# Kernel tuning notes

Hardware: AMD Instinct MI355X
Metric: run time of the kernel (lower is better)

Reference implementation:

```python
import jax, jax.numpy as jnp
import numpy as np

# Static multi-level feature-map shapes (H, W) per level.
SPATIAL_SHAPES = np.array([[92, 160], [46, 80], [23, 40], [12, 20]], dtype=np.int32)
NUM_HEADS = 8
NUM_LEVELS = 4
NUM_POINTS = 4      # sampling points per head per level (num_all_points)
NUM_Z = 4           # num_Z_anchors; NUM_POINTS % NUM_Z == 0
EMBED = 256
HEAD_DIM = EMBED // NUM_HEADS


def setup_inputs() -> dict:
    key = jax.random.key(0)
    ks = jax.random.split(key, 10)
    bs, nq = 2, 10000
    nv = int((SPATIAL_SHAPES[:, 0] * SPATIAL_SHAPES[:, 1]).sum())  # 19560
    query = jax.random.normal(ks[0], (bs, nq, EMBED), jnp.float32)
    value = jax.random.normal(ks[1], (bs, nv, EMBED), jnp.float32)
    query_pos = jax.random.normal(ks[2], (bs, nq, EMBED), jnp.float32)
    reference_points = jax.random.uniform(ks[3], (bs, nq, NUM_Z, 2), jnp.float32)
    W_val = jax.random.normal(ks[4], (EMBED, EMBED), jnp.float32) / jnp.sqrt(EMBED)
    b_val = jnp.zeros((EMBED,), jnp.float32)
    W_off = jax.random.normal(ks[5], (EMBED, NUM_HEADS * NUM_LEVELS * NUM_POINTS * 2), jnp.float32) * 0.01
    b_off = jax.random.normal(ks[6], (NUM_HEADS * NUM_LEVELS * NUM_POINTS * 2,), jnp.float32) * 0.5
    W_attn = jax.random.normal(ks[7], (EMBED, NUM_HEADS * NUM_LEVELS * NUM_POINTS), jnp.float32) * 0.02
    b_attn = jnp.zeros((NUM_HEADS * NUM_LEVELS * NUM_POINTS,), jnp.float32)
    spatial_shapes = jnp.asarray(SPATIAL_SHAPES)
    return {
        'query': query, 'value': value, 'query_pos': query_pos,
        'reference_points': reference_points,
        'W_val': W_val, 'b_val': b_val, 'W_off': W_off, 'b_off': b_off,
        'W_attn': W_attn, 'b_attn': b_attn, 'spatial_shapes': spatial_shapes,
    }


def _bilinear(v, x, y, H, W):
    """grid_sample(mode='bilinear', padding_mode='zeros', align_corners=False).

    v: (bs, H, W, heads, d); x, y: (bs, nq, heads, P) pixel coords.
    Returns (bs, nq, heads, P, d).
    """
    x0 = jnp.floor(x)
    y0 = jnp.floor(y)
    wx1 = x - x0
    wy1 = y - y0
    wx0 = 1.0 - wx1
    wy0 = 1.0 - wy1
    x0i = x0.astype(jnp.int32)
    y0i = y0.astype(jnp.int32)
    b = jnp.arange(v.shape[0])[:, None, None, None]
    h = jnp.arange(v.shape[3])[None, None, :, None]

    def gather(yi, xi):
        valid = (yi >= 0) & (yi < H) & (xi >= 0) & (xi < W)
        yc = jnp.clip(yi, 0, H - 1)
        xc = jnp.clip(xi, 0, W - 1)
        g = v[b, yc, xc, h]  # (bs, nq, heads, P, d)
        return g * valid[..., None].astype(v.dtype)

    return (gather(y0i, x0i) * (wy0 * wx0)[..., None]
            + gather(y0i, x0i + 1) * (wy0 * wx1)[..., None]
            + gather(y0i + 1, x0i) * (wy1 * wx0)[..., None]
            + gather(y0i + 1, x0i + 1) * (wy1 * wx1)[..., None])


def reference(query, value, query_pos, reference_points, W_val, b_val,
              W_off, b_off, W_attn, b_attn, spatial_shapes):
    bs, nq, _ = query.shape
    q = query + query_pos
    # value projection -> per-head values
    v = (value @ W_val + b_val).reshape(bs, -1, NUM_HEADS, HEAD_DIM)
    # sampling offsets and attention weights from query
    off = (q @ W_off + b_off).reshape(bs, nq, NUM_HEADS, NUM_LEVELS, NUM_POINTS, 2)
    attn = (q @ W_attn + b_attn).reshape(bs, nq, NUM_HEADS, NUM_LEVELS * NUM_POINTS)
    attn = jax.nn.softmax(attn, axis=-1).reshape(bs, nq, NUM_HEADS, NUM_LEVELS, NUM_POINTS)
    # normalize offsets by (w, h) of each level
    norm = jnp.stack([spatial_shapes[:, 1], spatial_shapes[:, 0]], -1).astype(q.dtype)  # (L, 2)
    off = off / norm[None, None, None, :, None, :]
    # fold Z-anchor reference points in, matching the shape[-1]==2 branch
    off = off.reshape(bs, nq, NUM_HEADS, NUM_LEVELS, NUM_POINTS // NUM_Z, NUM_Z, 2)
    loc = reference_points[:, :, None, None, None, :, :] + off
    loc = loc.reshape(bs, nq, NUM_HEADS, NUM_LEVELS, NUM_POINTS, 2)
    grid = 2.0 * loc - 1.0  # grid_sample convention

    start = 0
    sampled = []
    for lvl in range(NUM_LEVELS):
        H, W = int(SPATIAL_SHAPES[lvl, 0]), int(SPATIAL_SHAPES[lvl, 1])
        vl = v[:, start:start + H * W].reshape(bs, H, W, NUM_HEADS, HEAD_DIM)
        start += H * W
        # align_corners=False pixel coords
        x = ((grid[:, :, :, lvl, :, 0] + 1.0) * W - 1.0) * 0.5
        y = ((grid[:, :, :, lvl, :, 1] + 1.0) * H - 1.0) * 0.5
        sampled.append(_bilinear(vl, x, y, H, W))
    samp = jnp.stack(sampled, axis=3)  # (bs, nq, heads, L, P, d)
    out = (samp * attn[..., None]).sum(axis=(3, 4))  # (bs, nq, heads, d)
    return out.reshape(bs, nq, NUM_HEADS * HEAD_DIM)
```

## Files before the change

kernel.cpp:

```cpp
#include <hip/hip_runtime.h>
#include <hip/hip_fp16.h>

#define NQ 10000
#define BS 2
#define NV 19560
#define NH 8
#define HD 32
#define EMB 256

typedef __attribute__((ext_vector_type(8))) short bf16x8;
typedef __attribute__((ext_vector_type(4))) float f32x4;
typedef __attribute__((ext_vector_type(4))) short s16x4;

__device__ __forceinline__ unsigned short f2bf(float x) {
    unsigned u = __float_as_uint(x);
    u += 0x7FFFu + ((u >> 16) & 1u);
    return (unsigned short)(u >> 16);
}

__global__ __launch_bounds__(256) void convert_W(
    const float* __restrict__ Wv, const float* __restrict__ Wo,
    const float* __restrict__ Wa, const float* __restrict__ bv,
    const float* __restrict__ bo, const float* __restrict__ ba,
    ushort* __restrict__ Bt, float* __restrict__ bias) {
    int n = blockIdx.x;
    int k = threadIdx.x;
    float x;
    if (n < 256)       x = Wv[k * 256 + n];
    else if (n < 512)  x = Wo[k * 256 + (n - 256)];
    else               x = Wa[k * 128 + (n - 512)];
    Bt[n * 256 + k] = f2bf(x);
    if (k == 0)
        bias[n] = (n < 256) ? bv[n] : (n < 512) ? bo[n - 256] : ba[n - 512];
}

__global__ __launch_bounds__(256) void gemm_fused(
    const float* __restrict__ value, const float* __restrict__ query,
    const float* __restrict__ qpos, const ushort* __restrict__ Bt,
    const float* __restrict__ bias,
    ushort* __restrict__ Cv, float* __restrict__ C0, float* __restrict__ C1)
{
    __shared__ short As[64][40], Bhs[128][40];

    const int tid = threadIdx.x;

    const int bid0 = blockIdx.x;
    int bid;
    if (bid0 < 1224) {
        bid = (bid0 & 7) * 153 + (bid0 >> 3);
    } else {
        int q = bid0 - 1224;
        int xcd = q & 7, idx = q >> 3;
        int orig = (xcd < 3) ? (xcd * 118 + idx)
                             : (3 * 118 + (xcd - 3) * 117 + idx);
        bid = 1224 + orig;
    }

    bool isval; int mblk, npan;
    if (bid < 1224) { isval = true;  mblk = bid >> 1; npan = bid & 1; }
    else { int q = bid - 1224; isval = false; mblk = q / 3; npan = q % 3; }

    const int M  = isval ? (BS * NV) : (BS * NQ);
    const int m0 = mblk * 64;
    const int n0 = npan * 128;
    const int nbase = (isval ? 0 : 256) + n0;

    const float* A = isval ? value : query;

    const int arow = tid >> 2;
    const int acol = (tid & 3) * 8;
    const bool aval = (m0 + arow) < M;
    const float* Ap  = A    + (size_t)(m0 + arow) * 256 + acol;
    const float* A2p = qpos + (size_t)(m0 + arow) * 256 + acol;
    const int brow = tid >> 1;
    const int bcol = (tid & 1) * 16;
    const ushort* Bp = Bt + (size_t)(nbase + brow) * 256 + bcol;

    const int lane = tid & 63, wave = tid >> 6;
    const int wrow = (wave >> 1) * 32, wcol = (wave & 1) * 64;
    const int lr = lane & 15, quad = lane >> 4, lk = quad * 8;

    f32x4 acc[2][4] = {};

    for (int k0 = 0; k0 < 256; k0 += 32) {
        #pragma unroll
        for (int g = 0; g < 2; g++) {
            f32x4 v = {};
            if (aval) {
                v = *(const f32x4*)(Ap + k0 + g * 4);
                if (!isval) v += *(const f32x4*)(A2p + k0 + g * 4);
            }
            s16x4 hh;
            #pragma unroll
            for (int e = 0; e < 4; e++) hh[e] = (short)f2bf(v[e]);
            *(s16x4*)&As[arow][acol + g * 4] = hh;
        }
        *(bf16x8*)&Bhs[brow][bcol]     = *(const bf16x8*)(Bp + k0);
        *(bf16x8*)&Bhs[brow][bcol + 8] = *(const bf16x8*)(Bp + k0 + 8);
        __syncthreads();

        bf16x8 af[2], bhf[4];
        #pragma unroll
        for (int i = 0; i < 2; i++)
            af[i] = *(const bf16x8*)&As[wrow + i * 16 + lr][lk];
        #pragma unroll
        for (int j = 0; j < 4; j++)
            bhf[j] = *(const bf16x8*)&Bhs[wcol + j * 16 + lr][lk];
        #pragma unroll
        for (int i = 0; i < 2; i++)
            #pragma unroll
            for (int j = 0; j < 4; j++)
                acc[i][j] = __builtin_amdgcn_mfma_f32_16x16x32_bf16(af[i], bhf[j], acc[i][j], 0, 0, 0);
        __syncthreads();
    }

    #pragma unroll
    for (int j = 0; j < 4; j++) {
        int cc = wcol + j * 16 + lr;
        int col = n0 + cc;
        float bb = bias[nbase + cc];
        #pragma unroll
        for (int i = 0; i < 2; i++) {
            int gmb = m0 + wrow + i * 16 + quad * 4;
            #pragma unroll
            for (int r = 0; r < 4; r++) {
                int gm = gmb + r;
                if (gm < M) {
                    float val = acc[i][j][r] + bb;
                    if (isval) {
                        int h = col >> 5, d = col & 31;
                        int b = (gm >= NV) ? 1 : 0;
                        int pix = gm - b * NV;
                        Cv[((size_t)(b * 8 + h) * NV + pix) * 32 + d] =
                            __half_as_ushort(__float2half(val));
                    } else {
                        if (col < 256) C0[(size_t)gm * 256 + col] = val;
                        else           C1[(size_t)gm * 128 + (col - 256)] = val;
                    }
                }
            }
        }
    }
}

__global__ __launch_bounds__(256) void sample4(
    const ushort* __restrict__ v, const float* __restrict__ off,
    const float* __restrict__ attn, const float* __restrict__ refp,
    float* __restrict__ out)
{
    __shared__ int2 s_ow[256][4];

    const int t = threadIdx.x;
    const int combo = blockIdx.x & 15;
    const int qgrp  = blockIdx.x >> 4;
    const int b  = combo & 1;
    const int h0 = combo >> 1;

    {
        const int qloc = t >> 4;
        const int lp   = t & 15;
        const int l = lp >> 2, p = lp & 3;
        const size_t bq = (size_t)b * NQ + qgrp * 16 + qloc;

        float logit = attn[bq * 128 + h0 * 16 + lp];
        float mx = logit;
        #pragma unroll
        for (int m = 1; m < 16; m <<= 1) mx = fmaxf(mx, __shfl_xor(mx, m, 16));
        float e = __expf(logit - mx);
        float s = e;
        #pragma unroll
        for (int m = 1; m < 16; m <<= 1) s += __shfl_xor(s, m, 16);
        float w = e / s;

        const float Wf[4] = {160.f, 80.f, 40.f, 20.f};
        const float Hf[4] = {92.f, 46.f, 23.f, 12.f};
        const int   Wi[4] = {160, 80, 40, 20};
        const int   Hi[4] = {92, 46, 23, 12};
        const int   st[4] = {0, 14720, 18400, 19320};

        float ox = off[bq * 256 + h0 * 32 + l * 8 + p * 2];
        float oy = off[bq * 256 + h0 * 32 + l * 8 + p * 2 + 1];
        float rx = refp[bq * 8 + p * 2];
        float ry = refp[bq * 8 + p * 2 + 1];
        float x = rx * Wf[l] + ox - 0.5f;
        float y = ry * Hf[l] + oy - 0.5f;
        float x0f = floorf(x), y0f = floorf(y);
        float wx1 = x - x0f, wy1 = y - y0f;
        float wx0 = 1.f - wx1, wy0 = 1.f - wy1;
        int x0 = (int)x0f, y0 = (int)y0f;
        const int W = Wi[l], H = Hi[l];
        float mx0 = ((unsigned)x0       < (unsigned)W) ? 1.f : 0.f;
        float mx1 = ((unsigned)(x0 + 1) < (unsigned)W) ? 1.f : 0.f;
        float my0 = ((unsigned)y0       < (unsigned)H) ? 1.f : 0.f;
        float my1 = ((unsigned)(y0 + 1) < (unsigned)H) ? 1.f : 0.f;
        int xc0 = min(max(x0, 0), W - 1);
        int xc1 = min(max(x0 + 1, 0), W - 1);
        int yc0 = min(max(y0, 0), H - 1);
        int yc1 = min(max(y0 + 1, 0), H - 1);
        int base = ((b * 8 + h0) * NV + st[l]) * 32;
        s_ow[t][0] = make_int2(base + (yc0 * W + xc0) * 32,
                               __float_as_int(w * wy0 * wx0 * my0 * mx0));
        s_ow[t][1] = make_int2(base + (yc0 * W + xc1) * 32,
                               __float_as_int(w * wy0 * wx1 * my0 * mx1));
        s_ow[t][2] = make_int2(base + (yc1 * W + xc0) * 32,
                               __float_as_int(w * wy1 * wx0 * my1 * mx0));
        s_ow[t][3] = make_int2(base + (yc1 * W + xc1) * 32,
                               __float_as_int(w * wy1 * wx1 * my1 * mx1));
    }
    __syncthreads();

    const int g = t >> 4;
    const int lane = t & 15;
    const size_t bq = (size_t)b * NQ + qgrp * 16 + g;
    const int d2 = lane * 2;
    const int pbase = g * 16;

    float acc0 = 0.f, acc1 = 0.f, acc2 = 0.f, acc3 = 0.f;
    #pragma unroll
    for (int ib = 0; ib < 4; ib++) {
        int o[16]; float wgt[16];
        #pragma unroll
        for (int pp = 0; pp < 4; pp++) {
            int idx = pbase + ib * 4 + pp;
            #pragma unroll
            for (int c = 0; c < 4; c++) {
                int2 ow = s_ow[idx][c];
                o[pp * 4 + c]   = ow.x;
                wgt[pp * 4 + c] = __int_as_float(ow.y);
            }
        }
        unsigned u[16];
        #pragma unroll
        for (int j = 0; j < 16; j++)
            u[j] = *(const unsigned*)(v + o[j] + d2);
        #pragma unroll
        for (int j = 0; j < 16; j += 2) {
            float2 fa = __half22float2(*(const __half2*)&u[j]);
            float2 fb = __half22float2(*(const __half2*)&u[j + 1]);
            acc0 += wgt[j]     * fa.x;
            acc1 += wgt[j]     * fa.y;
            acc2 += wgt[j + 1] * fb.x;
            acc3 += wgt[j + 1] * fb.y;
        }
    }
    float2 res = make_float2(acc0 + acc2, acc1 + acc3);
    *(float2*)(out + bq * 256 + h0 * 32 + d2) = res;
}

extern "C" void kernel_launch(void* const* d_in, const int* in_sizes, int n_in,
                              void* d_out, int out_size, void* d_ws, size_t ws_size,
                              hipStream_t stream) {
    const float* query     = (const float*)d_in[0];
    const float* value     = (const float*)d_in[1];
    const float* query_pos = (const float*)d_in[2];
    const float* refp      = (const float*)d_in[3];
    const float* W_val     = (const float*)d_in[4];
    const float* b_val     = (const float*)d_in[5];
    const float* W_off     = (const float*)d_in[6];
    const float* b_off     = (const float*)d_in[7];
    const float* W_attn    = (const float*)d_in[8];
    const float* b_attn    = (const float*)d_in[9];
    float* out = (float*)d_out;

    char* w = (char*)d_ws;
    float*  off    = (float*)w;   w += 20480000;
    float*  attn   = (float*)w;   w += 10240000;
    ushort* vp_bf  = (ushort*)w;  w += 20029440;
    ushort* Bt     = (ushort*)w;  w += 327680;
    float*  bias_c = (float*)w;   w += 2560;

    convert_W<<<640, 256, 0, stream>>>(W_val, W_off, W_attn, b_val, b_off, b_attn,
                                       Bt, bias_c);

    gemm_fused<<<1224 + 939, 256, 0, stream>>>(value, query, query_pos, Bt, bias_c,
                                               vp_bf, off, attn);

    sample4<<<(BS * NQ / 16) * NH, 256, 0, stream>>>(vp_bf, off, attn, refp, out);
}
```

Before: 202.5 us.

## Remap sampling kernel to 64 queries per block with 16-byte gathers

The sampling kernel now gives each block 64 queries for one (batch, head) pair instead of 16. Each query gets 4 threads, and each thread handles one level's setup and 8 channels of the head dimension. Value gathers become 16-byte vector loads instead of 4-byte loads, and the setup uses vectorized float4 loads of logits, offsets and reference points. The shared table is padded to 65 columns to avoid bank conflicts, and a tail guard is added because 10000 is not a multiple of 64. In exchange, each thread issues more sequential gathers (64 points) and uses more registers.

```diff
diff --git a/kernel.cpp b/kernel.cpp
--- a/kernel.cpp
+++ b/kernel.cpp
@@ -9,6 +9,7 @@
 #define EMB 256
 
 typedef __attribute__((ext_vector_type(8))) short bf16x8;
+typedef __attribute__((ext_vector_type(8))) unsigned short u16x8;
 typedef __attribute__((ext_vector_type(4))) float f32x4;
 typedef __attribute__((ext_vector_type(4))) short s16x4;
 
@@ -148,7 +149,7 @@
     const float* __restrict__ attn, const float* __restrict__ refp,
     float* __restrict__ out)
 {
-    __shared__ int2 s_ow[256][4];
+    __shared__ int2 s_ow[64][65];
 
     const int t = threadIdx.x;
     const int combo = blockIdx.x & 15;
@@ -156,95 +157,112 @@
     const int b  = combo & 1;
     const int h0 = combo >> 1;
 
+    const int q = t >> 2;
+    const int l = t & 3;
+    const int qt = qgrp * 64 + q;
+    const bool valid = qt < NQ;
+    const size_t bq = (size_t)b * NQ + (valid ? qt : NQ - 1);
+
     {
-        const int qloc = t >> 4;
-        const int lp   = t & 15;
-        const int l = lp >> 2, p = lp & 3;
-        const size_t bq = (size_t)b * NQ + qgrp * 16 + qloc;
-
-        float logit = attn[bq * 128 + h0 * 16 + lp];
-        float mx = logit;
-        #pragma unroll
-        for (int m = 1; m < 16; m <<= 1) mx = fmaxf(mx, __shfl_xor(mx, m, 16));
-        float e = __expf(logit - mx);
-        float s = e;
-        #pragma unroll
-        for (int m = 1; m < 16; m <<= 1) s += __shfl_xor(s, m, 16);
-        float w = e / s;
-
-        const float Wf[4] = {160.f, 80.f, 40.f, 20.f};
-        const float Hf[4] = {92.f, 46.f, 23.f, 12.f};
-        const int   Wi[4] = {160, 80, 40, 20};
-        const int   Hi[4] = {92, 46, 23, 12};
-        const int   st[4] = {0, 14720, 18400, 19320};
-
-        float ox = off[bq * 256 + h0 * 32 + l * 8 + p * 2];
-        float oy = off[bq * 256 + h0 * 32 + l * 8 + p * 2 + 1];
-        float rx = refp[bq * 8 + p * 2];
-        float ry = refp[bq * 8 + p * 2 + 1];
-        float x = rx * Wf[l] + ox - 0.5f;
-        float y = ry * Hf[l] + oy - 0.5f;
-        float x0f = floorf(x), y0f = floorf(y);
-        float wx1 = x - x0f, wy1 = y - y0f;
-        float wx0 = 1.f - wx1, wy0 = 1.f - wy1;
-        int x0 = (int)x0f, y0 = (int)y0f;
-        const int W = Wi[l], H = Hi[l];
-        float mx0 = ((unsigned)x0       < (unsigned)W) ? 1.f : 0.f;
-        float mx1 = ((unsigned)(x0 + 1) < (unsigned)W) ? 1.f : 0.f;
-        float my0 = ((unsigned)y0       < (unsigned)H) ? 1.f : 0.f;
-        float my1 = ((unsigned)(y0 + 1) < (unsigned)H) ? 1.f : 0.f;
-        int xc0 = min(max(x0, 0), W - 1);
-        int xc1 = min(max(x0 + 1, 0), W - 1);
-        int yc0 = min(max(y0, 0), H - 1);
-        int yc1 = min(max(y0 + 1, 0), H - 1);
-        int base = ((b * 8 + h0) * NV + st[l]) * 32;
-        s_ow[t][0] = make_int2(base + (yc0 * W + xc0) * 32,
-                               __float_as_int(w * wy0 * wx0 * my0 * mx0));
-        s_ow[t][1] = make_int2(base + (yc0 * W + xc1) * 32,
-                               __float_as_int(w * wy0 * wx1 * my0 * mx1));
-        s_ow[t][2] = make_int2(base + (yc1 * W + xc0) * 32,
-                               __float_as_int(w * wy1 * wx0 * my1 * mx0));
-        s_ow[t][3] = make_int2(base + (yc1 * W + xc1) * 32,
-                               __float_as_int(w * wy1 * wx1 * my1 * mx1));
+        f32x4 lg = *(const f32x4*)(attn + bq * 128 + h0 * 16 + l * 4);
+        float mx = fmaxf(fmaxf(lg[0], lg[1]), fmaxf(lg[2], lg[3]));
+        mx = fmaxf(mx, __shfl_xor(mx, 1, 4));
+        mx = fmaxf(mx, __shfl_xor(mx, 2, 4));
+        float e0 = __expf(lg[0] - mx), e1 = __expf(lg[1] - mx);
+        float e2 = __expf(lg[2] - mx), e3 = __expf(lg[3] - mx);
+        float s = e0 + e1 + e2 + e3;
+        s += __shfl_xor(s, 1, 4);
+        s += __shfl_xor(s, 2, 4);
+        float inv = 1.f / s;
+
+        const float Wl = (l == 0) ? 160.f : (l == 1) ? 80.f : (l == 2) ? 40.f : 20.f;
+        const float Hl = (l == 0) ? 92.f  : (l == 1) ? 46.f : (l == 2) ? 23.f : 12.f;
+        const int  stl = (l == 0) ? 0 : (l == 1) ? 14720 : (l == 2) ? 18400 : 19320;
+        const int  Wi_ = (int)Wl, Hi_ = (int)Hl;
+        const int base = ((b * 8 + h0) * NV + stl) * 32;
+
+        f32x4 of0 = *(const f32x4*)(off + bq * 256 + h0 * 32 + l * 8);
+        f32x4 of1 = *(const f32x4*)(off + bq * 256 + h0 * 32 + l * 8 + 4);
+        f32x4 r0  = *(const f32x4*)(refp + bq * 8);
+        f32x4 r1  = *(const f32x4*)(refp + bq * 8 + 4);
+
+        float ws[4]  = {e0 * inv, e1 * inv, e2 * inv, e3 * inv};
+        float oxs[4] = {of0[0], of0[2], of1[0], of1[2]};
+        float oys[4] = {of0[1], of0[3], of1[1], of1[3]};
+        float rxs[4] = {r0[0], r0[2], r1[0], r1[2]};
+        float rys[4] = {r0[1], r0[3], r1[1], r1[3]};
+
+        #pragma unroll
+        for (int p = 0; p < 4; p++) {
+            float x = rxs[p] * Wl + oxs[p] - 0.5f;
+            float y = rys[p] * Hl + oys[p] - 0.5f;
+            float x0f = floorf(x), y0f = floorf(y);
+            float wx1 = x - x0f, wy1 = y - y0f;
+            float wx0 = 1.f - wx1, wy0 = 1.f - wy1;
+            int x0 = (int)x0f, y0 = (int)y0f;
+            float mx0 = ((unsigned)x0       < (unsigned)Wi_) ? 1.f : 0.f;
+            float mx1 = ((unsigned)(x0 + 1) < (unsigned)Wi_) ? 1.f : 0.f;
+            float my0 = ((unsigned)y0       < (unsigned)Hi_) ? 1.f : 0.f;
+            float my1 = ((unsigned)(y0 + 1) < (unsigned)Hi_) ? 1.f : 0.f;
+            int xc0 = min(max(x0, 0), Wi_ - 1);
+            int xc1 = min(max(x0 + 1, 0), Wi_ - 1);
+            int yc0 = min(max(y0, 0), Hi_ - 1);
+            int yc1 = min(max(y0 + 1, 0), Hi_ - 1);
+            float w = ws[p];
+            int pt4 = (l * 4 + p) * 4;
+            s_ow[q][pt4 + 0] = make_int2(base + (yc0 * Wi_ + xc0) * 32,
+                                         __float_as_int(w * wy0 * wx0 * my0 * mx0));
+            s_ow[q][pt4 + 1] = make_int2(base + (yc0 * Wi_ + xc1) * 32,
+                                         __float_as_int(w * wy0 * wx1 * my0 * mx1));
+            s_ow[q][pt4 + 2] = make_int2(base + (yc1 * Wi_ + xc0) * 32,
+                                         __float_as_int(w * wy1 * wx0 * my1 * mx0));
+            s_ow[q][pt4 + 3] = make_int2(base + (yc1 * Wi_ + xc1) * 32,
+                                         __float_as_int(w * wy1 * wx1 * my1 * mx1));
+        }
     }
     __syncthreads();
 
-    const int g = t >> 4;
-    const int lane = t & 15;
-    const size_t bq = (size_t)b * NQ + qgrp * 16 + g;
-    const int d2 = lane * 2;
-    const int pbase = g * 16;
-
-    float acc0 = 0.f, acc1 = 0.f, acc2 = 0.f, acc3 = 0.f;
+    const int d8 = l * 8;
+    const ushort* vb = v + d8;
+
+    float a0 = 0.f, a1 = 0.f, a2 = 0.f, a3 = 0.f;
+    float a4 = 0.f, a5 = 0.f, a6 = 0.f, a7 = 0.f;
+
     #pragma unroll
-    for (int ib = 0; ib < 4; ib++) {
-        int o[16]; float wgt[16];
-        #pragma unroll
-        for (int pp = 0; pp < 4; pp++) {
-            int idx = pbase + ib * 4 + pp;
-            #pragma unroll
-            for (int c = 0; c < 4; c++) {
-                int2 ow = s_ow[idx][c];
-                o[pp * 4 + c]   = ow.x;
-                wgt[pp * 4 + c] = __int_as_float(ow.y);
-            }
-        }
-        unsigned u[16];
-        #pragma unroll
-        for (int j = 0; j < 16; j++)
-            u[j] = *(const unsigned*)(v + o[j] + d2);
-        #pragma unroll
-        for (int j = 0; j < 16; j += 2) {
-            float2 fa = __half22float2(*(const __half2*)&u[j]);
-            float2 fb = __half22float2(*(const __half2*)&u[j + 1]);
-            acc0 += wgt[j]     * fa.x;
-            acc1 += wgt[j]     * fa.y;
-            acc2 += wgt[j + 1] * fb.x;
-            acc3 += wgt[j + 1] * fb.y;
-        }
-    }
-    float2 res = make_float2(acc0 + acc2, acc1 + acc3);
-    *(float2*)(out + bq * 256 + h0 * 32 + d2) = res;
+    for (int bt = 0; bt < 8; bt++) {
+        int2 ow[8];
+        #pragma unroll
+        for (int pp = 0; pp < 2; pp++)
+            #pragma unroll
+            for (int c = 0; c < 4; c++)
+                ow[pp * 4 + c] = s_ow[q][(bt * 2 + pp) * 4 + c];
+
+        u16x8 u[8];
+        #pragma unroll
+        for (int i = 0; i < 8; i++)
+            u[i] = *(const u16x8*)(vb + ow[i].x);
+
+        #pragma unroll
+        for (int i = 0; i < 8; i++) {
+            float w = __int_as_float(ow[i].y);
+            const __half2* hp = (const __half2*)&u[i];
+            float2 f0 = __half22float2(hp[0]);
+            float2 f1 = __half22float2(hp[1]);
+            float2 f2 = __half22float2(hp[2]);
+            float2 f3 = __half22float2(hp[3]);
+            a0 += w * f0.x; a1 += w * f0.y;
+            a2 += w * f1.x; a3 += w * f1.y;
+            a4 += w * f2.x; a5 += w * f2.y;
+            a6 += w * f3.x; a7 += w * f3.y;
+        }
+    }
+
+    if (valid) {
+        float* op = out + bq * 256 + h0 * 32 + d8;
+        f32x4 o0 = {a0, a1, a2, a3}, o1 = {a4, a5, a6, a7};
+        *(f32x4*)op       = o0;
+        *(f32x4*)(op + 4) = o1;
+    }
 }
 
 extern "C" void kernel_launch(void* const* d_in, const int* in_sizes, int n_in,
@@ -275,5 +293,5 @@
     gemm_fused<<<1224 + 939, 256, 0, stream>>>(value, query, query_pos, Bt, bias_c,
                                                vp_bf, off, attn);
 
-    sample4<<<(BS * NQ / 16) * NH, 256, 0, stream>>>(vp_bf, off, attn, refp, out);
-}
+    sample4<<<157 * 16, 256, 0, stream>>>(vp_bf, off, attn, refp, out);
+}
```

Result: no change. 199.8 us (-1.3%).
